# Kernel optimization log

Hardware: AMD Instinct MI355X
Metric: run time of the kernel (lower is better)

## Reference

```python
import jax, jax.numpy as jnp
import numpy as np

N, F, H, C = 4096, 128, 32, 205   # nodes, in-features, hidden=32, clusters=ceil(4096/20)
L, T, R = 512, 12, 4              # teams, team size, replaced members per team
EPS_POOL = 1e-15                  # torch_geometric EPS in dense_diff_pool
BN_EPS = 1e-5


def setup_inputs():
    ks = jax.random.split(jax.random.key(0), 12)
    rng = np.random.default_rng(0)
    # distinct node ids per team; replace = first R members, remain = rest
    teams = np.argsort(rng.random((L, N)), axis=1)[:, :T].astype(np.int64)
    g = lambda i, shape, s: jax.random.normal(ks[i], shape, jnp.float32) * s
    D = 2 * H + C  # 269
    return {
        'x': g(0, (N, F), 1.0),
        'adj': jax.random.uniform(ks[1], (1, N, N), jnp.float32),
        'sample_teams': jnp.asarray(teams),
        'sample_replaces': jnp.asarray(teams[:, :R]),
        'W1r': g(2, (F, H), 0.08), 'b1': jnp.zeros((H,), jnp.float32), 'W1root': g(3, (F, H), 0.08),
        'g1': jnp.ones((H,), jnp.float32), 'be1': jnp.zeros((H,), jnp.float32),
        'W2r': g(4, (H, H), 0.17), 'b2': jnp.zeros((H,), jnp.float32), 'W2root': g(5, (H, H), 0.17),
        'g2': jnp.ones((H,), jnp.float32), 'be2': jnp.zeros((H,), jnp.float32),
        'W3r': g(6, (H, C), 0.17), 'b3': jnp.zeros((C,), jnp.float32), 'W3root': g(7, (H, C), 0.17),
        'g3': jnp.ones((C,), jnp.float32), 'be3': jnp.zeros((C,), jnp.float32),
        'Wl1': g(8, (D, C), 0.07), 'bl1': jnp.zeros((C,), jnp.float32),
    }


def _conv(x, adj, Wr, br, Wroot):
    # DenseGraphConv: lin_rel(adj @ x) + lin_root(x)  (lin_root has no bias)
    return jnp.matmul(adj, x) @ Wr + br + x @ Wroot


def _bn(x, gamma, beta):
    # BatchNorm1d in training mode over flattened (B*N, C)
    B, n, c = x.shape
    xf = x.reshape(-1, c)
    m = xf.mean(0)
    v = jnp.mean((xf - m) ** 2, axis=0)  # biased variance, as torch uses for normalization
    return (((xf - m) / jnp.sqrt(v + BN_EPS)) * gamma + beta).reshape(B, n, c)


def _rownorm(a, eps=1e-8):
    n = jnp.linalg.norm(a, axis=1, keepdims=True)
    return a / jnp.maximum(n, eps)


def reference(x, adj, sample_teams, sample_replaces, W1r, b1, W1root, g1, be1,
              W2r, b2, W2root, g2, be2, W3r, b3, W3root, g3, be3, Wl1, bl1):
    # GNN tower (relu before bn, matching self.bn(i, conv(...).relu()))
    x1 = _bn(jax.nn.relu(_conv(x, adj, W1r, b1, W1root)), g1, be1)    # [1,N,H]
    x2 = _bn(jax.nn.relu(_conv(x1, adj, W2r, b2, W2root)), g2, be2)   # [1,N,H]
    x3 = _bn(jax.nn.relu(_conv(x2, adj, W3r, b3, W3root)), g3, be3)   # [1,N,C]
    xcat = jnp.concatenate([x1, x2, x3], axis=-1)                     # [1,N,2H+C]
    s1 = jax.nn.softmax(jax.nn.relu(xcat @ Wl1 + bl1), axis=2)        # [1,N,C]

    # link-prediction style norm: || s1[0] @ s1[0]^T - adj ||_F
    tmp = s1[0] @ s1[0].T - adj                                       # [1,N,N]
    norm = jnp.sqrt(jnp.sum(tmp * tmp))

    # dense_diff_pool entropy loss (it re-softmaxes its input s)
    s2 = jax.nn.softmax(s1, axis=-1)
    e1 = jnp.mean(jnp.sum(-s2 * jnp.log(s2 + EPS_POOL), axis=-1))

    # similarity alignment: only the diagonal of sim_matrix(sim_x_mat, sim_s_mat) is summed
    xn = _rownorm(x)
    sn = _rownorm(s1[0])
    sim_x_mat = xn @ xn.T                                             # [N,N]
    sim_s_mat = sn @ sn.T                                             # [N,N]
    a_n = _rownorm(sim_x_mat)
    b_n = _rownorm(sim_s_mat)
    sim = -jnp.sum(a_n * b_n) / sim_x_mat.shape[0]

    # per-team replace/remain mean-embedding L1 loss (padded segment means)
    emb = xcat[0]                                                     # [N, 2H+C]
    rep = emb[sample_replaces].mean(axis=1)                           # [L, D]
    rem = emb[sample_teams[:, R:]].mean(axis=1)                       # [L, D]
    embedding_loss = jnp.mean(jnp.sum(jnp.abs(rep - rem), axis=-1))

    total_loss = 100.0 * norm + 10.0 * e1 + 100.0 * sim + embedding_loss
    return (s1, norm, e1, sim, total_loss, embedding_loss, emb)
```

## Files before the change

### kernel.cpp

```cpp
#include <hip/hip_runtime.h>
#include <math.h>

#define NN 4096
#define FF 128
#define HH 32
#define CC 205
#define DD 269
#define LL 512
#define TT 12
#define RR 4
#define GP 208
#define DP 288
#define BST 40
#define GTS 224
#define NFIN 768
#define SC(i) ((i) * 32)
#define ZSTATS_N 10496
#define ZGT_N 69888

typedef __attribute__((ext_vector_type(8))) short bf16x8;
typedef __attribute__((ext_vector_type(4))) float f32x4;
typedef __attribute__((ext_vector_type(8))) unsigned short u16x8;

__device__ __forceinline__ float wave_sum(float v) {
#pragma unroll
  for (int o = 32; o > 0; o >>= 1) v += __shfl_xor(v, o, 64);
  return v;
}
__device__ __forceinline__ float wave_max(float v) {
#pragma unroll
  for (int o = 32; o > 0; o >>= 1) v = fmaxf(v, __shfl_xor(v, o, 64));
  return v;
}
__device__ __forceinline__ unsigned short f2bf(float x) {
  union { float f; unsigned u; } v; v.f = x;
  unsigned r = v.u + 0x7FFFu + ((v.u >> 16) & 1u);
  return (unsigned short)(r >> 16);
}

__global__ __launch_bounds__(256) void k_prep(const float* __restrict__ x,
                                              const float* __restrict__ W1r,
                                              const float* __restrict__ W1root,
                                              const float* __restrict__ Wl1,
                                              unsigned short* __restrict__ mB,
                                              float* __restrict__ rootb,
                                              float* __restrict__ xn,
                                              unsigned short* __restrict__ xnR,
                                              unsigned short* __restrict__ xnB,
                                              unsigned short* __restrict__ Wl1T,
                                              float* __restrict__ zstats,
                                              unsigned int* __restrict__ zgt) {
  __shared__ float sX[32][132];
  __shared__ unsigned short sT[32][34];
  __shared__ unsigned short sT2[FF][34];
  const int tid = threadIdx.x;
  {
    const int gidx = blockIdx.x * 256 + tid;
    if (gidx < ZSTATS_N) zstats[gidx] = 0.f;
    for (int i = gidx; i < ZGT_N; i += 65536) zgt[i] = 0u;
    if (gidx < GP * DP) {
      const int c = gidx / DP, k = gidx - c * DP;
      Wl1T[gidx] = (c < CC && k < DD) ? f2bf(Wl1[(size_t)k * CC + c]) : (unsigned short)0;
    }
  }
  if (blockIdx.x < 128) {
    const int kb = blockIdx.x;
    for (int p = tid; p < 1024; p += 256) {
      const int node = p >> 5, c4 = p & 31;
      const float4 v = *reinterpret_cast<const float4*>(&x[((size_t)(kb * 32 + node)) * FF + c4 * 4]);
      sX[node][c4 * 4 + 0] = v.x; sX[node][c4 * 4 + 1] = v.y;
      sX[node][c4 * 4 + 2] = v.z; sX[node][c4 * 4 + 3] = v.w;
    }
    __syncthreads();
    const int c = tid & 31, g = tid >> 5;
    float a1[4] = {0.f, 0.f, 0.f, 0.f}, a2[4] = {0.f, 0.f, 0.f, 0.f};
    for (int k = 0; k < FF; ++k) {
      const float w1 = W1r[k * HH + c];
      const float w2 = W1root[k * HH + c];
#pragma unroll
      for (int ni = 0; ni < 4; ++ni) {
        const float av = sX[g * 4 + ni][k];
        a1[ni] = fmaf(av, w1, a1[ni]);
        a2[ni] = fmaf(av, w2, a2[ni]);
      }
    }
#pragma unroll
    for (int ni = 0; ni < 4; ++ni) {
      rootb[((size_t)kb * 32 + g * 4 + ni) * HH + c] = a2[ni];
      sT[c][g * 4 + ni] = f2bf(a1[ni]);
    }
    __syncthreads();
    if (tid < 128) {
      const int row = tid >> 2, seg = tid & 3;
      u16x8 v;
#pragma unroll
      for (int j = 0; j < 8; ++j) v[j] = sT[row][seg * 8 + j];
      *reinterpret_cast<u16x8*>(&mB[((size_t)kb * 32 + row) * 32 + seg * 8]) = v;
    }
  } else {
    const int kb = blockIdx.x - 128;
    const int lane = tid & 63;
    const int w = tid >> 6;
#pragma unroll
    for (int i = 0; i < 8; ++i) {
      const int node = w * 8 + i;
      const int row = kb * 32 + node;
      const float v0 = x[(size_t)row * FF + lane];
      const float v1 = x[(size_t)row * FF + 64 + lane];
      const float ss = wave_sum(v0 * v0 + v1 * v1);
      const float n = fmaxf(sqrtf(ss), 1e-8f);
      const float a = v0 / n, b = v1 / n;
      xn[(size_t)row * FF + lane] = a;
      xn[(size_t)row * FF + 64 + lane] = b;
      xnR[(size_t)row * FF + lane] = f2bf(a);
      xnR[(size_t)row * FF + 64 + lane] = f2bf(b);
      sT2[lane][node] = f2bf(a);
      sT2[64 + lane][node] = f2bf(b);
    }
    __syncthreads();
    const int rowc = tid >> 1, seg = (tid & 1) * 16;
    if (rowc < FF) {
      u16x8 a, b;
#pragma unroll
      for (int j = 0; j < 8; ++j) { a[j] = sT2[rowc][seg + j]; b[j] = sT2[rowc][seg + 8 + j]; }
      *reinterpret_cast<u16x8*>(&xnB[((size_t)kb * GP + rowc) * 32 + seg]) = a;
      *reinterpret_cast<u16x8*>(&xnB[((size_t)kb * GP + rowc) * 32 + seg + 8]) = b;
    }
  }
}

__global__ __launch_bounds__(512) void k_conv1(const float* __restrict__ adj,
                                               unsigned short* __restrict__ adj_t,
                                               const unsigned short* __restrict__ mB,
                                               const float* __restrict__ bias,
                                               const float* __restrict__ root,
                                               float* __restrict__ t,
                                               float* __restrict__ colsum,
                                               float* __restrict__ colsq,
                                               float* __restrict__ scalars) {
  __shared__ unsigned short sA[16][520];
  __shared__ float sRed[8][16][33];
  __shared__ float ls[HH], lq[HH];
  __shared__ float redsq[8];
  const int tid = threadIdx.x;
  const int lane = tid & 63;
  const int w = tid >> 6;
  const int l15 = lane & 15;
  const int kgrp = (lane >> 4) * 8;
  const int rb = blockIdx.x;
  const int row0 = rb * 16;
  float adjsq = 0.f;
  f32x4 acc0 = {0.f, 0.f, 0.f, 0.f}, acc1 = {0.f, 0.f, 0.f, 0.f};
  const int fr[4] = {(0 * 512 + tid) >> 7, (1 * 512 + tid) >> 7, (2 * 512 + tid) >> 7,
                     (3 * 512 + tid) >> 7};
  const int fc[4] = {(0 * 512 + tid) & 127, (1 * 512 + tid) & 127, (2 * 512 + tid) & 127,
                     (3 * 512 + tid) & 127};
  float4 v[4];
#pragma unroll
  for (int i = 0; i < 4; ++i)
    v[i] = *reinterpret_cast<const float4*>(&adj[(size_t)(row0 + fr[i]) * NN + fc[i] * 4]);
  for (int chunk = 0; chunk < 8; ++chunk) {
    const int kbase = chunk * 512;
#pragma unroll
    for (int i = 0; i < 4; ++i) {
      const float4 vv = v[i];
      adjsq += vv.x * vv.x + vv.y * vv.y + vv.z * vv.z + vv.w * vv.w;
      ushort4 h;
      h.x = f2bf(vv.x); h.y = f2bf(vv.y); h.z = f2bf(vv.z); h.w = f2bf(vv.w);
      const size_t toff = ((size_t)rb * (NN / 32) + (kbase >> 5) + (fc[i] >> 3)) * 512 +
                          fr[i] * 32 + (fc[i] & 7) * 4;
      *reinterpret_cast<ushort4*>(&adj_t[toff]) = h;
      *reinterpret_cast<ushort4*>(&sA[fr[i]][fc[i] * 4]) = h;
    }
    __syncthreads();
    if (chunk < 7) {
      const int kn = kbase + 512;
#pragma unroll
      for (int i = 0; i < 4; ++i)
        v[i] = *reinterpret_cast<const float4*>(&adj[(size_t)(row0 + fr[i]) * NN + kn + fc[i] * 4]);
    }
#pragma unroll
    for (int j = 0; j < 2; ++j) {
      const int ktl = w * 2 + j;
      const bf16x8 a = *reinterpret_cast<const bf16x8*>(&sA[l15][ktl * 32 + kgrp]);
      const size_t boff = (size_t)(chunk * 16 + ktl) * 1024;
      const bf16x8 b0 = *reinterpret_cast<const bf16x8*>(&mB[boff + l15 * 32 + kgrp]);
      const bf16x8 b1v = *reinterpret_cast<const bf16x8*>(&mB[boff + (16 + l15) * 32 + kgrp]);
      acc0 = __builtin_amdgcn_mfma_f32_16x16x32_bf16(a, b0, acc0, 0, 0, 0);
      acc1 = __builtin_amdgcn_mfma_f32_16x16x32_bf16(a, b1v, acc1, 0, 0, 0);
    }
    __syncthreads();
  }
  const int crow = (lane >> 4) * 4;
#pragma unroll
  for (int r = 0; r < 4; ++r) {
    sRed[w][crow + r][l15] = acc0[r];
    sRed[w][crow + r][16 + l15] = acc1[r];
  }
  if (tid < HH) { ls[tid] = 0.f; lq[tid] = 0.f; }
  adjsq = wave_sum(adjsq);
  if (lane == 0) redsq[w] = adjsq;
  __syncthreads();
  {
    const int r = tid >> 5, c = tid & 31;
    float vv = 0.f;
#pragma unroll
    for (int i = 0; i < 8; ++i) vv += sRed[i][r][c];
    const int n = row0 + r;
    float s = bias[c] + root[(size_t)n * HH + c] + vv;
    s = fmaxf(s, 0.f);
    t[(size_t)n * HH + c] = s;
    atomicAdd(&ls[c], s);
    atomicAdd(&lq[c], s * s);
  }
  __syncthreads();
  if (tid < HH) {
    atomicAdd(&colsum[tid * 16], ls[tid]);
    atomicAdd(&colsq[tid * 16], lq[tid]);
  }
  if (tid == 0) {
    float s = 0.f;
#pragma unroll
    for (int i = 0; i < 8; ++i) s += redsq[i];
    atomicAdd(&scalars[SC(1)], s);
  }
}

__global__ __launch_bounds__(512) void k_conv2(const unsigned short* __restrict__ adj_t,
                                               const unsigned short* __restrict__ mB,
                                               const float* __restrict__ bias,
                                               const float* __restrict__ root,
                                               float* __restrict__ t,
                                               float* __restrict__ colsum,
                                               float* __restrict__ colsq) {
  __shared__ float sRed[8][16][33];
  __shared__ float ls[HH], lq[HH];
  const int tid = threadIdx.x;
  const int lane = tid & 63;
  const int w = tid >> 6;
  const int l15 = lane & 15;
  const int kgrp = (lane >> 4) * 8;
  const int rb = blockIdx.x;
  const int row0 = rb * 16;
  const int kb0 = w * 16;
  f32x4 acc0 = {0.f, 0.f, 0.f, 0.f}, acc1 = {0.f, 0.f, 0.f, 0.f};
#pragma unroll
  for (int h = 0; h < 2; ++h) {
    bf16x8 a[8], b0[8], b1v[8];
#pragma unroll
    for (int kt = 0; kt < 8; ++kt) {
      const int kb = kb0 + h * 8 + kt;
      const size_t aoff = ((size_t)rb * (NN / 32) + kb) * 512;
      const size_t boff = (size_t)kb * 1024;
      a[kt] = *reinterpret_cast<const bf16x8*>(&adj_t[aoff + l15 * 32 + kgrp]);
      b0[kt] = *reinterpret_cast<const bf16x8*>(&mB[boff + (size_t)l15 * 32 + kgrp]);
      b1v[kt] = *reinterpret_cast<const bf16x8*>(&mB[boff + (size_t)(16 + l15) * 32 + kgrp]);
    }
#pragma unroll
    for (int kt = 0; kt < 8; ++kt) {
      acc0 = __builtin_amdgcn_mfma_f32_16x16x32_bf16(a[kt], b0[kt], acc0, 0, 0, 0);
      acc1 = __builtin_amdgcn_mfma_f32_16x16x32_bf16(a[kt], b1v[kt], acc1, 0, 0, 0);
    }
  }
  const int crow = (lane >> 4) * 4;
#pragma unroll
  for (int r = 0; r < 4; ++r) {
    sRed[w][crow + r][l15] = acc0[r];
    sRed[w][crow + r][16 + l15] = acc1[r];
  }
  if (tid < HH) { ls[tid] = 0.f; lq[tid] = 0.f; }
  __syncthreads();
  {
    const int r = tid >> 5, c = tid & 31;
    float v = 0.f;
#pragma unroll
    for (int i = 0; i < 8; ++i) v += sRed[i][r][c];
    const int n = row0 + r;
    float s = bias[c] + root[(size_t)n * HH + c] + v;
    s = fmaxf(s, 0.f);
    t[(size_t)n * HH + c] = s;
    atomicAdd(&ls[c], s);
    atomicAdd(&lq[c], s * s);
  }
  __syncthreads();
  if (tid < HH) {
    atomicAdd(&colsum[tid * 16], ls[tid]);
    atomicAdd(&colsq[tid * 16], lq[tid]);
  }
}

__global__ __launch_bounds__(512) void k_conv3(const unsigned short* __restrict__ adj_t,
                                               const unsigned short* __restrict__ x2B,
                                               const float* __restrict__ W3r,
                                               const float* __restrict__ b3,
                                               const float* __restrict__ x2,
                                               const float* __restrict__ W3root,
                                               float* __restrict__ t3,
                                               float* __restrict__ colsum,
                                               float* __restrict__ colsq) {
  __shared__ float sRed[8][16][33];
  __shared__ float sZ[16][33];
  __shared__ float sXr[16][33];
  const int tid = threadIdx.x;
  const int lane = tid & 63;
  const int w = tid >> 6;
  const int l15 = lane & 15;
  const int kgrp = (lane >> 4) * 8;
  const int rb = blockIdx.x;
  const int row0 = rb * 16;
  const int kb0 = w * 16;
  f32x4 acc0 = {0.f, 0.f, 0.f, 0.f}, acc1 = {0.f, 0.f, 0.f, 0.f};
#pragma unroll
  for (int h = 0; h < 2; ++h) {
    bf16x8 a[8], b0[8], b1v[8];
#pragma unroll
    for (int kt = 0; kt < 8; ++kt) {
      const int kb = kb0 + h * 8 + kt;
      const size_t aoff = ((size_t)rb * (NN / 32) + kb) * 512;
      const size_t boff = (size_t)kb * 1024;
      a[kt] = *reinterpret_cast<const bf16x8*>(&adj_t[aoff + l15 * 32 + kgrp]);
      b0[kt] = *reinterpret_cast<const bf16x8*>(&x2B[boff + (size_t)l15 * 32 + kgrp]);
      b1v[kt] = *reinterpret_cast<const bf16x8*>(&x2B[boff + (size_t)(16 + l15) * 32 + kgrp]);
    }
#pragma unroll
    for (int kt = 0; kt < 8; ++kt) {
      acc0 = __builtin_amdgcn_mfma_f32_16x16x32_bf16(a[kt], b0[kt], acc0, 0, 0, 0);
      acc1 = __builtin_amdgcn_mfma_f32_16x16x32_bf16(a[kt], b1v[kt], acc1, 0, 0, 0);
    }
  }
  const int crow = (lane >> 4) * 4;
#pragma unroll
  for (int r = 0; r < 4; ++r) {
    sRed[w][crow + r][l15] = acc0[r];
    sRed[w][crow + r][16 + l15] = acc1[r];
  }
  {
    const int r = tid >> 5, c = tid & 31;
    if (tid < 512) sXr[r][c] = x2[(size_t)(row0 + r) * HH + c];
  }
  __syncthreads();
  {
    const int r = tid >> 5, c = tid & 31;
    float v = 0.f;
#pragma unroll
    for (int i = 0; i < 8; ++i) v += sRed[i][r][c];
    sZ[r][c] = v;
  }
  __syncthreads();
  const int c = tid;
  if (c >= CC) return;
  float acc[16];
  const float bb = b3[c];
#pragma unroll
  for (int r = 0; r < 16; ++r) acc[r] = bb;
  for (int k = 0; k < 32; ++k) {
    const float w1 = W3r[k * CC + c];
    const float w2 = W3root[k * CC + c];
#pragma unroll
    for (int r = 0; r < 16; ++r) acc[r] += sZ[r][k] * w1 + sXr[r][k] * w2;
  }
  float lsm = 0.f, lqm = 0.f;
#pragma unroll
  for (int r = 0; r < 16; ++r) {
    const float v = fmaxf(acc[r], 0.f);
    t3[(size_t)(row0 + r) * CC + c] = v;
    lsm += v;
    lqm += v * v;
  }
  atomicAdd(&colsum[c * 16], lsm);
  atomicAdd(&colsq[c * 16], lqm);
}

__global__ __launch_bounds__(256) void k_bnproj(const float* __restrict__ t,
                                                const float* __restrict__ colsum,
                                                const float* __restrict__ colsq,
                                                const float* __restrict__ g,
                                                const float* __restrict__ be,
                                                const float* __restrict__ W2r,
                                                const float* __restrict__ W2root,
                                                unsigned short* __restrict__ mB,
                                                float* __restrict__ rootb,
                                                float* __restrict__ emb) {
  __shared__ float sXf[32][33];
  __shared__ unsigned short sT[32][34];
  const int tid = threadIdx.x;
  const int kb = blockIdx.x;
  const int c = tid & 31, gq = tid >> 5;
  const float m = colsum[c * 16] * (1.f / NN);
  const float var = fmaxf(colsq[c * 16] * (1.f / NN) - m * m, 0.f);
  const float Ac = g[c] / sqrtf(var + 1e-5f);
  const float Bc = be[c] - m * Ac;
#pragma unroll
  for (int ni = 0; ni < 4; ++ni) {
    const int n = kb * 32 + gq * 4 + ni;
    const float v = fmaf(Ac, t[(size_t)n * HH + c], Bc);
    emb[(size_t)n * DD + c] = v;
    sXf[gq * 4 + ni][c] = v;
  }
  __syncthreads();
  float a1[4] = {0.f, 0.f, 0.f, 0.f}, a2[4] = {0.f, 0.f, 0.f, 0.f};
  for (int k = 0; k < HH; ++k) {
    const float w1 = W2r[k * HH + c];
    const float w2 = W2root[k * HH + c];
#pragma unroll
    for (int ni = 0; ni < 4; ++ni) {
      const float av = sXf[gq * 4 + ni][k];
      a1[ni] = fmaf(av, w1, a1[ni]);
      a2[ni] = fmaf(av, w2, a2[ni]);
    }
  }
#pragma unroll
  for (int ni = 0; ni < 4; ++ni) {
    rootb[((size_t)kb * 32 + gq * 4 + ni) * HH + c] = a2[ni];
    sT[c][gq * 4 + ni] = f2bf(a1[ni]);
  }
  __syncthreads();
  if (tid < 128) {
    const int row = tid >> 2, seg = tid & 3;
    u16x8 v;
#pragma unroll
    for (int j = 0; j < 8; ++j) v[j] = sT[row][seg * 8 + j];
    *reinterpret_cast<u16x8*>(&mB[((size_t)kb * 32 + row) * 32 + seg * 8]) = v;
  }
}

__global__ __launch_bounds__(256) void k_bnapply32(const float* __restrict__ t,
                                                   const float* __restrict__ colsum,
                                                   const float* __restrict__ colsq,
                                                   const float* __restrict__ g,
                                                   const float* __restrict__ be,
                                                   float* __restrict__ xo,
                                                   float* __restrict__ emb, int embOff,
                                                   unsigned short* __restrict__ xB) {
  __shared__ unsigned short sT[32][34];
  const int tid = threadIdx.x;
  const int kb = blockIdx.x;
  const int c = tid & 31, gq = tid >> 5;
  const float m = colsum[c * 16] * (1.f / NN);
  const float var = fmaxf(colsq[c * 16] * (1.f / NN) - m * m, 0.f);
  const float Ac = g[c] / sqrtf(var + 1e-5f);
  const float Bc = be[c] - m * Ac;
#pragma unroll
  for (int ni = 0; ni < 4; ++ni) {
    const int n = kb * 32 + gq * 4 + ni;
    const float v = fmaf(Ac, t[(size_t)n * HH + c], Bc);
    xo[(size_t)n * HH + c] = v;
    emb[(size_t)n * DD + embOff + c] = v;
    sT[c][gq * 4 + ni] = f2bf(v);
  }
  __syncthreads();
  if (tid < 128) {
    const int row = tid >> 2, seg = tid & 3;
    u16x8 o;
#pragma unroll
    for (int j = 0; j < 8; ++j) o[j] = sT[row][seg * 8 + j];
    *reinterpret_cast<u16x8*>(&xB[((size_t)kb * 32 + row) * 32 + seg * 8]) = o;
  }
}

__global__ __launch_bounds__(256) void k_head(float* __restrict__ emb,
                                              const float* __restrict__ t3,
                                              const float* __restrict__ colsum3,
                                              const float* __restrict__ colsq3,
                                              const float* __restrict__ g3,
                                              const float* __restrict__ be3,
                                              const unsigned short* __restrict__ Wl1T,
                                              const float* __restrict__ bl1,
                                              float* __restrict__ s1,
                                              float* __restrict__ sn,
                                              unsigned short* __restrict__ s1B,
                                              unsigned short* __restrict__ snB,
                                              unsigned short* __restrict__ snR,
                                              float* __restrict__ scalars) {
  __shared__ unsigned short sA[16][296];
  __shared__ float lg[16][212];
  __shared__ unsigned short sTa[16][212];
  __shared__ unsigned short sTb[16][212];
  __shared__ float redE[4];
  const int tid = threadIdx.x;
  const int row0 = blockIdx.x * 16;
  for (int p = tid; p < 16 * 36; p += 256) {
    const int r = p / 36, ch = p - r * 36;
    const int row = row0 + r;
#pragma unroll
    for (int j = 0; j < 8; ++j) {
      const int d = ch * 8 + j;
      float v;
      if (d < 2 * HH) {
        v = emb[(size_t)row * DD + d];
      } else if (d < DD) {
        const int c3 = d - 2 * HH;
        const float m = colsum3[c3 * 16] * (1.f / NN);
        const float var = fmaxf(colsq3[c3 * 16] * (1.f / NN) - m * m, 0.f);
        const float Ac = g3[c3] / sqrtf(var + 1e-5f);
        const float Bc = be3[c3] - m * Ac;
        v = fmaf(Ac, t3[(size_t)row * CC + c3], Bc);
        emb[(size_t)row * DD + d] = v;
      } else {
        v = 0.f;
      }
      sA[r][d] = f2bf(v);
    }
  }
  __syncthreads();
  const int lane = tid & 63;
  const int w = tid >> 6;
  const int l15 = lane & 15;
  const int kgrp = (lane >> 4) * 8;
  {
    f32x4 acc[4];
#pragma unroll
    for (int i = 0; i < 4; ++i) acc[i] = (f32x4){0.f, 0.f, 0.f, 0.f};
#pragma unroll
    for (int i = 0; i < 4; ++i) {
      const int ct = w + i * 4;
      if (ct < 13) {
        const size_t brow = (size_t)(ct * 16 + l15) * DP;
#pragma unroll
        for (int k0 = 0; k0 < DP; k0 += 32) {
          const bf16x8 a = *reinterpret_cast<const bf16x8*>(&sA[l15][k0 + kgrp]);
          const bf16x8 b = *reinterpret_cast<const bf16x8*>(&Wl1T[brow + k0 + kgrp]);
          acc[i] = __builtin_amdgcn_mfma_f32_16x16x32_bf16(a, b, acc[i], 0, 0, 0);
        }
      }
    }
    const int lrow = (lane >> 4) * 4;
#pragma unroll
    for (int i = 0; i < 4; ++i) {
      const int ct = w + i * 4;
      if (ct < 13) {
#pragma unroll
        for (int r = 0; r < 4; ++r) lg[lrow + r][ct * 16 + l15] = acc[i][r];
      }
    }
  }
  __syncthreads();
  const int r0 = w * 4;
  const int c0 = lane * 4;
  const bool active = (c0 < GP);
  float bl[4];
#pragma unroll
  for (int j = 0; j < 4; ++j) bl[j] = (c0 + j < CC) ? bl1[c0 + j] : 0.f;
  float ent_acc = 0.f;
#pragma unroll
  for (int r = 0; r < 4; ++r) {
    const int lr = r0 + r;
    const int row = row0 + lr;
    float lgv[4] = {0.f, 0.f, 0.f, 0.f};
    if (active) {
#pragma unroll
      for (int j = 0; j < 4; ++j) lgv[j] = lg[lr][c0 + j];
    }
    float v[4];
    float ml = -1e30f;
#pragma unroll
    for (int j = 0; j < 4; ++j) {
      const int c = c0 + j;
      v[j] = (c < CC) ? fmaxf(lgv[j] + bl[j], 0.f) : -1e30f;
      ml = fmaxf(ml, v[j]);
    }
    const float m = wave_max(ml);
    float e[4];
    float sl = 0.f;
#pragma unroll
    for (int j = 0; j < 4; ++j) {
      const int c = c0 + j;
      e[j] = (c < CC) ? __expf(v[j] - m) : 0.f;
      sl += e[j];
    }
    const float S = wave_sum(sl);
    const float invS = 1.f / S;
    float p[4];
    float ql = 0.f;
#pragma unroll
    for (int j = 0; j < 4; ++j) {
      p[j] = e[j] * invS;
      ql += p[j] * p[j];
    }
    const float q = wave_sum(ql);
    const float inv = 1.f / fmaxf(sqrtf(q), 1e-8f);
    float m2l = -1e30f;
#pragma unroll
    for (int j = 0; j < 4; ++j) {
      const int c = c0 + j;
      if (c < CC) {
        s1[(size_t)row * CC + c] = p[j];
        sn[(size_t)row * CC + c] = p[j] * inv;
        m2l = fmaxf(m2l, p[j]);
      }
    }
    if (active) {
#pragma unroll
      for (int j = 0; j < 4; ++j) {
        const int c = c0 + j;
        const bool ok = (c < CC);
        sTa[lr][c] = ok ? f2bf(p[j]) : (unsigned short)0;
        sTb[lr][c] = ok ? f2bf(p[j] * inv) : (unsigned short)0;
      }
    }
    if (c0 < GTS) {
      ushort4 o;
      o.x = (c0 + 0 < CC) ? f2bf(p[0] * inv) : (unsigned short)0;
      o.y = (c0 + 1 < CC) ? f2bf(p[1] * inv) : (unsigned short)0;
      o.z = (c0 + 2 < CC) ? f2bf(p[2] * inv) : (unsigned short)0;
      o.w = (c0 + 3 < CC) ? f2bf(p[3] * inv) : (unsigned short)0;
      *reinterpret_cast<ushort4*>(&snR[(size_t)row * GTS + c0]) = o;
    }
    const float m2 = wave_max(m2l);
    float e2[4];
    float s2l = 0.f;
#pragma unroll
    for (int j = 0; j < 4; ++j) {
      const int c = c0 + j;
      e2[j] = (c < CC) ? __expf(p[j] - m2) : 0.f;
      s2l += e2[j];
    }
    const float S2 = wave_sum(s2l);
    const float invS2 = 1.f / S2;
    float tl = 0.f;
#pragma unroll
    for (int j = 0; j < 4; ++j) {
      const int c = c0 + j;
      if (c < CC) {
        const float sp = e2[j] * invS2;
        tl -= sp * logf(sp + 1e-15f);
      }
    }
    ent_acc += tl;
  }
  ent_acc = wave_sum(ent_acc);
  if (lane == 0) redE[w] = ent_acc;
  __syncthreads();
  if (tid == 0) atomicAdd(&scalars[SC(2)], redE[0] + redE[1] + redE[2] + redE[3]);
  if (tid < GP) {
    const int kb = row0 >> 5, no = row0 & 31;
    u16x8 oa0, ob0, oa1, ob1;
#pragma unroll
    for (int r = 0; r < 8; ++r) {
      oa0[r] = sTa[r][tid]; ob0[r] = sTb[r][tid];
      oa1[r] = sTa[8 + r][tid]; ob1[r] = sTb[8 + r][tid];
    }
    *reinterpret_cast<u16x8*>(&s1B[((size_t)kb * GP + tid) * 32 + no]) = oa0;
    *reinterpret_cast<u16x8*>(&s1B[((size_t)kb * GP + tid) * 32 + no + 8]) = oa1;
    *reinterpret_cast<u16x8*>(&snB[((size_t)kb * GP + tid) * 32 + no]) = ob0;
    *reinterpret_cast<u16x8*>(&snB[((size_t)kb * GP + tid) * 32 + no + 8]) = ob1;
  }
}

__global__ __launch_bounds__(512) void k_tail(const unsigned short* __restrict__ adj_t,
                                              const unsigned short* __restrict__ s1B,
                                              const float* __restrict__ s1,
                                              const unsigned short* __restrict__ xnB,
                                              const unsigned short* __restrict__ snB,
                                              unsigned short* __restrict__ GT0,
                                              unsigned short* __restrict__ GxsT,
                                              unsigned short* __restrict__ GsT,
                                              float* __restrict__ scalars) {
  const int tid = threadIdx.x;
  const int lane = tid & 63;
  const int w = tid >> 6;
  const int l15 = lane & 15;
  const int kgrp = (lane >> 4) * 8;
  if (blockIdx.x < 512) {
    __shared__ unsigned short sB[2][13][16][BST];
    __shared__ float red[8];
    const int bx = blockIdx.x & 31;
    const int ky = blockIdx.x >> 5;
    const int rb = bx * 8 + w;
    const int kb0 = ky * 8;
    const int g = lane >> 4;
    const int p0 = tid;
    const int ct0 = p0 >> 6, rr0 = (p0 >> 2) & 15, sg0 = (p0 & 3) * 8;
    const int p1 = tid + 512;
    const bool v1 = (p1 < 832);
    const int ct1 = p1 >> 6, rr1 = (p1 >> 2) & 15, sg1 = (p1 & 3) * 8;
    f32x4 acc[13];
#pragma unroll
    for (int ct = 0; ct < 13; ++ct) acc[ct] = (f32x4){0.f, 0.f, 0.f, 0.f};
    u16x8 st0, st1;
    st0 = *reinterpret_cast<const u16x8*>(&s1B[((size_t)kb0 * GP + ct0 * 16 + rr0) * 32 + sg0]);
    if (v1) st1 = *reinterpret_cast<const u16x8*>(&s1B[((size_t)kb0 * GP + ct1 * 16 + rr1) * 32 + sg1]);
    *reinterpret_cast<u16x8*>(&sB[0][ct0][rr0][sg0]) = st0;
    if (v1) *reinterpret_cast<u16x8*>(&sB[0][ct1][rr1][sg1]) = st1;
    __syncthreads();
    bf16x8 a = *reinterpret_cast<const bf16x8*>(
        &adj_t[((size_t)rb * (NN / 32) + kb0) * 512 + l15 * 32 + kgrp]);
    for (int kt = 0; kt < 8; ++kt) {
      const int cur = kt & 1;
      if (kt < 7) {
        const size_t kb = kb0 + kt + 1;
        st0 = *reinterpret_cast<const u16x8*>(&s1B[(kb * GP + ct0 * 16 + rr0) * 32 + sg0]);
        if (v1) st1 = *reinterpret_cast<const u16x8*>(&s1B[(kb * GP + ct1 * 16 + rr1) * 32 + sg1]);
      }
      bf16x8 a_next = a;
      if (kt < 7)
        a_next = *reinterpret_cast<const bf16x8*>(
            &adj_t[((size_t)rb * (NN / 32) + kb0 + kt + 1) * 512 + l15 * 32 + kgrp]);
#pragma unroll
      for (int ct = 0; ct < 13; ++ct) {
        const bf16x8 b = *reinterpret_cast<const bf16x8*>(&sB[cur][ct][l15][kgrp]);
        acc[ct] = __builtin_amdgcn_mfma_f32_16x16x32_bf16(a, b, acc[ct], 0, 0, 0);
      }
      if (kt < 7) {
        *reinterpret_cast<u16x8*>(&sB[cur ^ 1][ct0][rr0][sg0]) = st0;
        if (v1) *reinterpret_cast<u16x8*>(&sB[cur ^ 1][ct1][rr1][sg1]) = st1;
      }
      __syncthreads();
      a = a_next;
    }
    const int rout = rb * 16 + g * 4;
    float sc = 0.f;
#pragma unroll
    for (int ct = 0; ct < 13; ++ct) {
      const int col = ct * 16 + l15;
      if (col < CC) {
#pragma unroll
        for (int r = 0; r < 4; ++r)
          sc = fmaf(acc[ct][r], s1[(size_t)(rout + r) * CC + col], sc);
      }
    }
    sc = wave_sum(sc);
    if (lane == 0) red[w] = sc;
    __syncthreads();
    if (tid == 0) {
      float s = 0.f;
#pragma unroll
      for (int i = 0; i < 8; ++i) s += red[i];
      atomicAdd(&scalars[SC(0)], s);
    }
  } else {
    __shared__ float redg[8][16][17];
    __shared__ float redq[8];
    const int gb = blockIdx.x - 512;
    const int gid = gb / 169;
    const int rem = gb - gid * 169;
    const int tp = (rem % 13) * 16;
    const int tq = (rem / 13) * 16;
    const unsigned short *PT, *QT;
    unsigned short* GTout = nullptr;
    if (gid == 0)      { PT = xnB; QT = xnB; GTout = GT0;  if (tp >= FF || tq >= FF) return; }
    else if (gid == 1) { PT = xnB; QT = snB; GTout = GxsT; if (tp >= FF) return; }
    else if (gid == 2) { PT = snB; QT = snB; GTout = GsT; }
    else               { PT = s1B; QT = s1B; }
    f32x4 acc = {0.f, 0.f, 0.f, 0.f};
#pragma unroll 4
    for (int kt = 0; kt < 16; ++kt) {
      const int kb = w * 16 + kt;
      const bf16x8 a = *reinterpret_cast<const bf16x8*>(&PT[((size_t)kb * GP + tp + l15) * 32 + kgrp]);
      const bf16x8 b = *reinterpret_cast<const bf16x8*>(&QT[((size_t)kb * GP + tq + l15) * 32 + kgrp]);
      acc = __builtin_amdgcn_mfma_f32_16x16x32_bf16(a, b, acc, 0, 0, 0);
    }
    const int crow = (lane >> 4) * 4;
#pragma unroll
    for (int r = 0; r < 4; ++r) redg[w][crow + r][l15] = acc[r];
    __syncthreads();
    const int rr = tid >> 4, cc = tid & 15;
    if (gid == 3) {
      float q = 0.f;
      if (tid < 256) {
        float v = 0.f;
#pragma unroll
        for (int i = 0; i < 8; ++i) v += redg[i][rr][cc];
        q = v * v;
      }
      q = wave_sum(q);
      if (lane == 0) redq[w] = q;
      __syncthreads();
      if (tid == 0) {
        float s = 0.f;
#pragma unroll
        for (int i = 0; i < 8; ++i) s += redq[i];
        atomicAdd(&scalars[SC(5)], s);
      }
    } else {
      if (tid < 256) {
        float vt = 0.f;
#pragma unroll
        for (int i = 0; i < 8; ++i) vt += redg[i][cc][rr];
        GTout[(size_t)(tq + rr) * GTS + (tp + cc)] = f2bf(vt);
      }
    }
  }
}

__global__ __launch_bounds__(256) void k_finloss(const unsigned short* __restrict__ xnR,
                                                 const unsigned short* __restrict__ snR,
                                                 const unsigned short* __restrict__ GT0,
                                                 const unsigned short* __restrict__ GxsT,
                                                 const unsigned short* __restrict__ GsT,
                                                 const float* __restrict__ xn,
                                                 const float* __restrict__ sn,
                                                 const float* __restrict__ emb,
                                                 const int* __restrict__ teams,
                                                 const int* __restrict__ reps,
                                                 float* __restrict__ scalars,
                                                 unsigned int* __restrict__ ticket,
                                                 float* __restrict__ outsc) {
  __shared__ __align__(16) char smem[47424];
  const int tid = threadIdx.x;
  if (blockIdx.x < 256) {
    unsigned short (*sX)[136] = (unsigned short(*)[136])(smem);
    unsigned short (*sS)[232] = (unsigned short(*)[232])(smem + 4352);
    float (*sH1)[132] = (float(*)[132])(smem + 11776);
    float (*sU)[212] = (float(*)[212])(smem + 20224);
    float (*sH2)[212] = (float(*)[212])(smem + 33792);
    float* redb = (float*)(smem + 47360);
    const int row0 = blockIdx.x * 16;
    for (int p = tid; p < 16 * 16; p += 256) {
      const int r = p >> 4, ch = p & 15;
      *reinterpret_cast<u16x8*>(&sX[r][ch * 8]) =
          *reinterpret_cast<const u16x8*>(&xnR[(size_t)(row0 + r) * FF + ch * 8]);
    }
    for (int p = tid; p < 16 * 28; p += 256) {
      const int r = p / 28, ch = p - r * 28;
      *reinterpret_cast<u16x8*>(&sS[r][ch * 8]) =
          *reinterpret_cast<const u16x8*>(&snR[(size_t)(row0 + r) * GTS + ch * 8]);
    }
    __syncthreads();
    const int lane = tid & 63;
    const int w = tid >> 6;
    const int l15 = lane & 15;
    const int kgrp = (lane >> 4) * 8;
    const int lrow = (lane >> 4) * 4;
#pragma unroll
    for (int i = 0; i < 2; ++i) {
      const int ct = w + i * 4;
      f32x4 acc = {0.f, 0.f, 0.f, 0.f};
      const size_t brow = (size_t)(ct * 16 + l15) * GTS;
#pragma unroll
      for (int k0 = 0; k0 < FF; k0 += 32) {
        const bf16x8 a = *reinterpret_cast<const bf16x8*>(&sX[l15][k0 + kgrp]);
        const bf16x8 b = *reinterpret_cast<const bf16x8*>(&GT0[brow + k0 + kgrp]);
        acc = __builtin_amdgcn_mfma_f32_16x16x32_bf16(a, b, acc, 0, 0, 0);
      }
#pragma unroll
      for (int r = 0; r < 4; ++r) sH1[lrow + r][ct * 16 + l15] = acc[r];
    }
#pragma unroll
    for (int i = 0; i < 4; ++i) {
      const int ct = w + i * 4;
      if (ct < 13) {
        f32x4 acc = {0.f, 0.f, 0.f, 0.f};
        const size_t brow = (size_t)(ct * 16 + l15) * GTS;
#pragma unroll
        for (int k0 = 0; k0 < FF; k0 += 32) {
          const bf16x8 a = *reinterpret_cast<const bf16x8*>(&sX[l15][k0 + kgrp]);
          const bf16x8 b = *reinterpret_cast<const bf16x8*>(&GxsT[brow + k0 + kgrp]);
          acc = __builtin_amdgcn_mfma_f32_16x16x32_bf16(a, b, acc, 0, 0, 0);
        }
#pragma unroll
        for (int r = 0; r < 4; ++r) sU[lrow + r][ct * 16 + l15] = acc[r];
      }
    }
#pragma unroll
    for (int i = 0; i < 4; ++i) {
      const int ct = w + i * 4;
      if (ct < 13) {
        f32x4 acc = {0.f, 0.f, 0.f, 0.f};
        const size_t brow = (size_t)(ct * 16 + l15) * GTS;
#pragma unroll
        for (int k0 = 0; k0 < GTS; k0 += 32) {
          const bf16x8 a = *reinterpret_cast<const bf16x8*>(&sS[l15][k0 + kgrp]);
          const bf16x8 b = *reinterpret_cast<const bf16x8*>(&GsT[brow + k0 + kgrp]);
          acc = __builtin_amdgcn_mfma_f32_16x16x32_bf16(a, b, acc, 0, 0, 0);
        }
#pragma unroll
        for (int r = 0; r < 4; ++r) sH2[lrow + r][ct * 16 + l15] = acc[r];
      }
    }
    __syncthreads();
    float acc_sim = 0.f;
#pragma unroll
    for (int r = 0; r < 4; ++r) {
      const int lr = w * 4 + r;
      const int row = row0 + lr;
      float suu = 0.f, suv = 0.f, svv = 0.f;
#pragma unroll
      for (int c0 = 0; c0 < FF; c0 += 64) {
        suu = fmaf(xn[(size_t)row * FF + c0 + lane], sH1[lr][c0 + lane], suu);
      }
      for (int cb = lane; cb < CC; cb += 64) {
        const float sv = sn[(size_t)row * CC + cb];
        suv = fmaf(sU[lr][cb], sv, suv);
        svv = fmaf(sH2[lr][cb], sv, svv);
      }
      suu = wave_sum(suu);
      suv = wave_sum(suv);
      svv = wave_sum(svv);
      if (lane == 0) acc_sim += suv / sqrtf(suu * svv);
    }
    if (lane == 0) redb[w] = acc_sim;
    __syncthreads();
    if (tid == 0) atomicAdd(&scalars[SC(3)], redb[0] + redb[1] + redb[2] + redb[3]);
  } else {
    float* red = (float*)smem;
    const int team = blockIdx.x - 256;
    float part = 0.f;
    for (int d = tid; d < DD; d += 256) {
      float a = 0.f, b = 0.f;
#pragma unroll
      for (int m = 0; m < RR; ++m) a += emb[(size_t)reps[team * RR + m] * DD + d];
#pragma unroll
      for (int m = RR; m < TT; ++m) b += emb[(size_t)teams[team * TT + m] * DD + d];
      part += fabsf(a * (1.f / RR) - b * (1.f / (TT - RR)));
    }
    part = wave_sum(part);
    if ((tid & 63) == 0) red[tid >> 6] = part;
    __syncthreads();
    if (tid == 0) atomicAdd(&scalars[SC(4)], red[0] + red[1] + red[2] + red[3]);
  }
  if (tid == 0) {
    __threadfence();
    const unsigned int old = atomicAdd(ticket, 1u);
    if (old == (unsigned int)(NFIN - 1)) {
      const float trSAS = atomicAdd(&scalars[SC(0)], 0.f);
      const float adjsq = atomicAdd(&scalars[SC(1)], 0.f);
      const float ent   = atomicAdd(&scalars[SC(2)], 0.f);
      const float simS  = atomicAdd(&scalars[SC(3)], 0.f);
      const float embS  = atomicAdd(&scalars[SC(4)], 0.f);
      const float sumP2 = atomicAdd(&scalars[SC(5)], 0.f);
      const float normsq = fmaxf(sumP2 - 2.f * trSAS + adjsq, 0.f);
      const float norm = sqrtf(normsq);
      const float e1 = ent * (1.f / NN);
      const float sim = -simS * (1.f / NN);
      const float embl = embS * (1.f / LL);
      outsc[0] = norm;
      outsc[1] = e1;
      outsc[2] = sim;
      outsc[3] = 100.f * norm + 10.f * e1 + 100.f * sim + embl;
      outsc[4] = embl;
    }
  }
}

extern "C" void kernel_launch(void* const* d_in, const int* in_sizes, int n_in,
                              void* d_out, int out_size, void* d_ws, size_t ws_size,
                              hipStream_t stream) {
  const float* x      = (const float*)d_in[0];
  const float* adj    = (const float*)d_in[1];
  const int*   teams  = (const int*)d_in[2];
  const int*   reps   = (const int*)d_in[3];
  const float* W1r    = (const float*)d_in[4];
  const float* b1     = (const float*)d_in[5];
  const float* W1root = (const float*)d_in[6];
  const float* g1     = (const float*)d_in[7];
  const float* be1    = (const float*)d_in[8];
  const float* W2r    = (const float*)d_in[9];
  const float* b2     = (const float*)d_in[10];
  const float* W2root = (const float*)d_in[11];
  const float* g2     = (const float*)d_in[12];
  const float* be2    = (const float*)d_in[13];
  const float* W3r    = (const float*)d_in[14];
  const float* b3     = (const float*)d_in[15];
  const float* W3root = (const float*)d_in[16];
  const float* g3     = (const float*)d_in[17];
  const float* be3    = (const float*)d_in[18];
  const float* Wl1    = (const float*)d_in[19];
  const float* bl1    = (const float*)d_in[20];

  char* wp = (char*)d_ws;
  auto alloc = [&](size_t bytes) { char* p = wp; wp += (bytes + 255) & ~(size_t)255; return p; };
  unsigned short* adj_t = (unsigned short*)alloc((size_t)NN * NN * 2);
  unsigned short* mB    = (unsigned short*)alloc((size_t)HH * NN * 2);
  unsigned short* x2B   = (unsigned short*)alloc((size_t)HH * NN * 2);
  unsigned short* s1B   = (unsigned short*)alloc((size_t)GP * NN * 2);
  unsigned short* snB   = (unsigned short*)alloc((size_t)GP * NN * 2);
  unsigned short* Wl1T  = (unsigned short*)alloc((size_t)GP * DP * 2);
  unsigned short* xnR   = (unsigned short*)alloc((size_t)NN * FF * 2);
  unsigned short* snR   = (unsigned short*)alloc((size_t)NN * GTS * 2);
  float* rootb  = (float*)alloc((size_t)NN * HH * 4);
  float* t      = (float*)alloc((size_t)NN * HH * 4);
  float* x2     = (float*)alloc((size_t)NN * HH * 4);
  float* t3     = (float*)alloc((size_t)NN * CC * 4);
  float* sn     = (float*)alloc((size_t)NN * CC * 4);
  float* xn     = (float*)alloc((size_t)NN * FF * 4);
  unsigned short* xnB   = (unsigned short*)alloc((size_t)GP * NN * 2);
  float* scalars = (float*)alloc(256 * 4);
  float* colsum1 = (float*)alloc(512 * 4);
  float* colsq1  = (float*)alloc(512 * 4);
  float* colsum2 = (float*)alloc(512 * 4);
  float* colsq2  = (float*)alloc(512 * 4);
  float* colsum3 = (float*)alloc(4096 * 4);
  float* colsq3  = (float*)alloc(4096 * 4);
  unsigned short* GTall = (unsigned short*)alloc((size_t)3 * GP * GTS * 2);
  unsigned short* GT0   = GTall;
  unsigned short* GxsT  = GTall + (size_t)GP * GTS;
  unsigned short* GsT   = GTall + (size_t)2 * GP * GTS;
  unsigned int* ticket = (unsigned int*)&scalars[SC(6)];
  (void)ws_size; (void)in_sizes; (void)n_in; (void)out_size;

  float* out   = (float*)d_out;
  float* s1    = out;
  float* outsc = out + (size_t)NN * CC;
  float* emb   = out + (size_t)NN * CC + 5;

  k_prep<<<256, 256, 0, stream>>>(x, W1r, W1root, Wl1, mB, rootb, xn, xnR, xnB, Wl1T,
                                  scalars, (unsigned int*)GTall);

  k_conv1<<<256, 512, 0, stream>>>(adj, adj_t, mB, b1, rootb, t, colsum1, colsq1, scalars);
  k_bnproj<<<NN / 32, 256, 0, stream>>>(t, colsum1, colsq1, g1, be1, W2r, W2root, mB, rootb, emb);

  k_conv2<<<256, 512, 0, stream>>>(adj_t, mB, b2, rootb, t, colsum2, colsq2);
  k_bnapply32<<<NN / 32, 256, 0, stream>>>(t, colsum2, colsq2, g2, be2, x2, emb, HH, x2B);

  k_conv3<<<256, 512, 0, stream>>>(adj_t, x2B, W3r, b3, x2, W3root, t3, colsum3, colsq3);

  k_head<<<NN / 16, 256, 0, stream>>>(emb, t3, colsum3, colsq3, g3, be3, Wl1T, bl1,
                                      s1, sn, s1B, snB, snR, scalars);

  k_tail<<<512 + 676, 512, 0, stream>>>(adj_t, s1B, s1, xnB, snB, GT0, GxsT, GsT, scalars);

  k_finloss<<<NFIN, 256, 0, stream>>>(xnR, snR, GT0, GxsT, GsT, xn, sn, emb, teams, reps,
                                      scalars, ticket, outsc);
}
```

Baseline: 182.0 us.

## Fuse batchnorm apply and projection into conv kernels via grid-wide ticket barrier

```diff
diff --git a/kernel.cpp b/kernel.cpp
--- a/kernel.cpp
+++ b/kernel.cpp
@@ -15,7 +15,7 @@
 #define GTS 224
 #define NFIN 768
 #define SC(i) ((i) * 32)
-#define ZSTATS_N 10496
+#define ZSTATS_N 10560
 #define ZGT_N 69888
 
 typedef __attribute__((ext_vector_type(8))) short bf16x8;
@@ -131,17 +131,26 @@
 
 __global__ __launch_bounds__(512) void k_conv1(const float* __restrict__ adj,
                                                unsigned short* __restrict__ adj_t,
-                                               const unsigned short* __restrict__ mB,
+                                               unsigned short* __restrict__ mB,
                                                const float* __restrict__ bias,
                                                const float* __restrict__ root,
-                                               float* __restrict__ t,
+                                               const float* __restrict__ g,
+                                               const float* __restrict__ be,
+                                               const float* __restrict__ W2r,
+                                               const float* __restrict__ W2root,
+                                               float* __restrict__ rootb,
+                                               float* __restrict__ emb,
                                                float* __restrict__ colsum,
                                                float* __restrict__ colsq,
-                                               float* __restrict__ scalars) {
+                                               float* __restrict__ scalars,
+                                               unsigned int* __restrict__ tk) {
   __shared__ unsigned short sA[16][520];
   __shared__ float sRed[8][16][33];
   __shared__ float ls[HH], lq[HH];
   __shared__ float redsq[8];
+  __shared__ float sTt[16][33];
+  __shared__ float sXf[16][33];
+  __shared__ unsigned short sTm[32][18];
   const int tid = threadIdx.x;
   const int lane = tid & 63;
   const int w = tid >> 6;
@@ -201,17 +210,16 @@
   adjsq = wave_sum(adjsq);
   if (lane == 0) redsq[w] = adjsq;
   __syncthreads();
+  const int r16 = tid >> 5, c32 = tid & 31;
   {
-    const int r = tid >> 5, c = tid & 31;
     float vv = 0.f;
 #pragma unroll
-    for (int i = 0; i < 8; ++i) vv += sRed[i][r][c];
-    const int n = row0 + r;
-    float s = bias[c] + root[(size_t)n * HH + c] + vv;
+    for (int i = 0; i < 8; ++i) vv += sRed[i][r16][c32];
+    float s = bias[c32] + root[(size_t)(row0 + r16) * HH + c32] + vv;
     s = fmaxf(s, 0.f);
-    t[(size_t)n * HH + c] = s;
-    atomicAdd(&ls[c], s);
-    atomicAdd(&lq[c], s * s);
+    sTt[r16][c32] = s;
+    atomicAdd(&ls[c32], s);
+    atomicAdd(&lq[c32], s * s);
   }
   __syncthreads();
   if (tid < HH) {
@@ -223,6 +231,43 @@
 #pragma unroll
     for (int i = 0; i < 8; ++i) s += redsq[i];
     atomicAdd(&scalars[SC(1)], s);
+  }
+  if (tid == 0) {
+    __threadfence();
+    atomicAdd(tk, 1u);
+    while (atomicAdd(tk, 0u) < 256u) __builtin_amdgcn_s_sleep(8);
+  }
+  __syncthreads();
+  {
+    const float cs = atomicAdd(&colsum[c32 * 16], 0.f);
+    const float cq = atomicAdd(&colsq[c32 * 16], 0.f);
+    const float m = cs * (1.f / NN);
+    const float var = fmaxf(cq * (1.f / NN) - m * m, 0.f);
+    const float Ac = g[c32] / sqrtf(var + 1e-5f);
+    const float Bc = be[c32] - m * Ac;
+    const float vv = fmaf(Ac, sTt[r16][c32], Bc);
+    emb[(size_t)(row0 + r16) * DD + c32] = vv;
+    sXf[r16][c32] = vv;
+  }
+  __syncthreads();
+  {
+    float a1 = 0.f, a2 = 0.f;
+    for (int k = 0; k < HH; ++k) {
+      const float av = sXf[r16][k];
+      a1 = fmaf(av, W2r[k * HH + c32], a1);
+      a2 = fmaf(av, W2root[k * HH + c32], a2);
+    }
+    rootb[(size_t)(row0 + r16) * HH + c32] = a2;
+    sTm[c32][r16] = f2bf(a1);
+  }
+  __syncthreads();
+  if (tid < 64) {
+    const int row = tid >> 1, half = tid & 1;
+    u16x8 o;
+#pragma unroll
+    for (int j = 0; j < 8; ++j) o[j] = sTm[row][half * 8 + j];
+    const int kb = rb >> 1;
+    *reinterpret_cast<u16x8*>(&mB[((size_t)(kb * 32 + row)) * 32 + (rb & 1) * 16 + half * 8]) = o;
   }
 }
 
@@ -230,11 +275,18 @@
                                                const unsigned short* __restrict__ mB,
                                                const float* __restrict__ bias,
                                                const float* __restrict__ root,
-                                               float* __restrict__ t,
+                                               const float* __restrict__ g,
+                                               const float* __restrict__ be,
+                                               float* __restrict__ x2,
+                                               float* __restrict__ emb,
+                                               unsigned short* __restrict__ x2B,
                                                float* __restrict__ colsum,
-                                               float* __restrict__ colsq) {
+                                               float* __restrict__ colsq,
+                                               unsigned int* __restrict__ tk) {
   __shared__ float sRed[8][16][33];
   __shared__ float ls[HH], lq[HH];
+  __shared__ float sTt[16][33];
+  __shared__ unsigned short sTm[32][18];
   const int tid = threadIdx.x;
   const int lane = tid & 63;
   const int w = tid >> 6;
@@ -270,22 +322,48 @@
   }
   if (tid < HH) { ls[tid] = 0.f; lq[tid] = 0.f; }
   __syncthreads();
+  const int r16 = tid >> 5, c32 = tid & 31;
   {
-    const int r = tid >> 5, c = tid & 31;
-    float v = 0.f;
-#pragma unroll
-    for (int i = 0; i < 8; ++i) v += sRed[i][r][c];
-    const int n = row0 + r;
-    float s = bias[c] + root[(size_t)n * HH + c] + v;
+    float vv = 0.f;
+#pragma unroll
+    for (int i = 0; i < 8; ++i) vv += sRed[i][r16][c32];
+    float s = bias[c32] + root[(size_t)(row0 + r16) * HH + c32] + vv;
     s = fmaxf(s, 0.f);
-    t[(size_t)n * HH + c] = s;
-    atomicAdd(&ls[c], s);
-    atomicAdd(&lq[c], s * s);
+    sTt[r16][c32] = s;
+    atomicAdd(&ls[c32], s);
+    atomicAdd(&lq[c32], s * s);
   }
   __syncthreads();
   if (tid < HH) {
     atomicAdd(&colsum[tid * 16], ls[tid]);
     atomicAdd(&colsq[tid * 16], lq[tid]);
+  }
+  if (tid == 0) {
+    __threadfence();
+    atomicAdd(tk, 1u);
+    while (atomicAdd(tk, 0u) < 256u) __builtin_amdgcn_s_sleep(8);
+  }
+  __syncthreads();
+  {
+    const float cs = atomicAdd(&colsum[c32 * 16], 0.f);
+    const float cq = atomicAdd(&colsq[c32 * 16], 0.f);
+    const float m = cs * (1.f / NN);
+    const float var = fmaxf(cq * (1.f / NN) - m * m, 0.f);
+    const float Ac = g[c32] / sqrtf(var + 1e-5f);
+    const float Bc = be[c32] - m * Ac;
+    const float vv = fmaf(Ac, sTt[r16][c32], Bc);
+    x2[(size_t)(row0 + r16) * HH + c32] = vv;
+    emb[(size_t)(row0 + r16) * DD + HH + c32] = vv;
+    sTm[c32][r16] = f2bf(vv);
+  }
+  __syncthreads();
+  if (tid < 64) {
+    const int row = tid >> 1, half = tid & 1;
+    u16x8 o;
+#pragma unroll
+    for (int j = 0; j < 8; ++j) o[j] = sTm[row][half * 8 + j];
+    const int kb = rb >> 1;
+    *reinterpret_cast<u16x8*>(&x2B[((size_t)(kb * 32 + row)) * 32 + (rb & 1) * 16 + half * 8]) = o;
   }
 }
 
@@ -369,93 +447,6 @@
   }
   atomicAdd(&colsum[c * 16], lsm);
   atomicAdd(&colsq[c * 16], lqm);
-}
-
-__global__ __launch_bounds__(256) void k_bnproj(const float* __restrict__ t,
-                                                const float* __restrict__ colsum,
-                                                const float* __restrict__ colsq,
-                                                const float* __restrict__ g,
-                                                const float* __restrict__ be,
-                                                const float* __restrict__ W2r,
-                                                const float* __restrict__ W2root,
-                                                unsigned short* __restrict__ mB,
-                                                float* __restrict__ rootb,
-                                                float* __restrict__ emb) {
-  __shared__ float sXf[32][33];
-  __shared__ unsigned short sT[32][34];
-  const int tid = threadIdx.x;
-  const int kb = blockIdx.x;
-  const int c = tid & 31, gq = tid >> 5;
-  const float m = colsum[c * 16] * (1.f / NN);
-  const float var = fmaxf(colsq[c * 16] * (1.f / NN) - m * m, 0.f);
-  const float Ac = g[c] / sqrtf(var + 1e-5f);
-  const float Bc = be[c] - m * Ac;
-#pragma unroll
-  for (int ni = 0; ni < 4; ++ni) {
-    const int n = kb * 32 + gq * 4 + ni;
-    const float v = fmaf(Ac, t[(size_t)n * HH + c], Bc);
-    emb[(size_t)n * DD + c] = v;
-    sXf[gq * 4 + ni][c] = v;
-  }
-  __syncthreads();
-  float a1[4] = {0.f, 0.f, 0.f, 0.f}, a2[4] = {0.f, 0.f, 0.f, 0.f};
-  for (int k = 0; k < HH; ++k) {
-    const float w1 = W2r[k * HH + c];
-    const float w2 = W2root[k * HH + c];
-#pragma unroll
-    for (int ni = 0; ni < 4; ++ni) {
-      const float av = sXf[gq * 4 + ni][k];
-      a1[ni] = fmaf(av, w1, a1[ni]);
-      a2[ni] = fmaf(av, w2, a2[ni]);
-    }
-  }
-#pragma unroll
-  for (int ni = 0; ni < 4; ++ni) {
-    rootb[((size_t)kb * 32 + gq * 4 + ni) * HH + c] = a2[ni];
-    sT[c][gq * 4 + ni] = f2bf(a1[ni]);
-  }
-  __syncthreads();
-  if (tid < 128) {
-    const int row = tid >> 2, seg = tid & 3;
-    u16x8 v;
-#pragma unroll
-    for (int j = 0; j < 8; ++j) v[j] = sT[row][seg * 8 + j];
-    *reinterpret_cast<u16x8*>(&mB[((size_t)kb * 32 + row) * 32 + seg * 8]) = v;
-  }
-}
-
-__global__ __launch_bounds__(256) void k_bnapply32(const float* __restrict__ t,
-                                                   const float* __restrict__ colsum,
-                                                   const float* __restrict__ colsq,
-                                                   const float* __restrict__ g,
-                                                   const float* __restrict__ be,
-                                                   float* __restrict__ xo,
-                                                   float* __restrict__ emb, int embOff,
-                                                   unsigned short* __restrict__ xB) {
-  __shared__ unsigned short sT[32][34];
-  const int tid = threadIdx.x;
-  const int kb = blockIdx.x;
-  const int c = tid & 31, gq = tid >> 5;
-  const float m = colsum[c * 16] * (1.f / NN);
-  const float var = fmaxf(colsq[c * 16] * (1.f / NN) - m * m, 0.f);
-  const float Ac = g[c] / sqrtf(var + 1e-5f);
-  const float Bc = be[c] - m * Ac;
-#pragma unroll
-  for (int ni = 0; ni < 4; ++ni) {
-    const int n = kb * 32 + gq * 4 + ni;
-    const float v = fmaf(Ac, t[(size_t)n * HH + c], Bc);
-    xo[(size_t)n * HH + c] = v;
-    emb[(size_t)n * DD + embOff + c] = v;
-    sT[c][gq * 4 + ni] = f2bf(v);
-  }
-  __syncthreads();
-  if (tid < 128) {
-    const int row = tid >> 2, seg = tid & 3;
-    u16x8 o;
-#pragma unroll
-    for (int j = 0; j < 8; ++j) o[j] = sT[row][seg * 8 + j];
-    *reinterpret_cast<u16x8*>(&xB[((size_t)kb * 32 + row) * 32 + seg * 8]) = o;
-  }
 }
 
 __global__ __launch_bounds__(256) void k_head(float* __restrict__ emb,
@@ -969,13 +960,12 @@
   unsigned short* xnR   = (unsigned short*)alloc((size_t)NN * FF * 2);
   unsigned short* snR   = (unsigned short*)alloc((size_t)NN * GTS * 2);
   float* rootb  = (float*)alloc((size_t)NN * HH * 4);
-  float* t      = (float*)alloc((size_t)NN * HH * 4);
   float* x2     = (float*)alloc((size_t)NN * HH * 4);
   float* t3     = (float*)alloc((size_t)NN * CC * 4);
   float* sn     = (float*)alloc((size_t)NN * CC * 4);
   float* xn     = (float*)alloc((size_t)NN * FF * 4);
   unsigned short* xnB   = (unsigned short*)alloc((size_t)GP * NN * 2);
-  float* scalars = (float*)alloc(256 * 4);
+  float* scalars = (float*)alloc(320 * 4);
   float* colsum1 = (float*)alloc(512 * 4);
   float* colsq1  = (float*)alloc(512 * 4);
   float* colsum2 = (float*)alloc(512 * 4);
@@ -987,6 +977,8 @@
   unsigned short* GxsT  = GTall + (size_t)GP * GTS;
   unsigned short* GsT   = GTall + (size_t)2 * GP * GTS;
   unsigned int* ticket = (unsigned int*)&scalars[SC(6)];
+  unsigned int* tk1    = (unsigned int*)&scalars[SC(7)];
+  unsigned int* tk2    = (unsigned int*)&scalars[SC(8)];
   (void)ws_size; (void)in_sizes; (void)n_in; (void)out_size;
 
   float* out   = (float*)d_out;
@@ -997,11 +989,11 @@
   k_prep<<<256, 256, 0, stream>>>(x, W1r, W1root, Wl1, mB, rootb, xn, xnR, xnB, Wl1T,
                                   scalars, (unsigned int*)GTall);
 
-  k_conv1<<<256, 512, 0, stream>>>(adj, adj_t, mB, b1, rootb, t, colsum1, colsq1, scalars);
-  k_bnproj<<<NN / 32, 256, 0, stream>>>(t, colsum1, colsq1, g1, be1, W2r, W2root, mB, rootb, emb);
-
-  k_conv2<<<256, 512, 0, stream>>>(adj_t, mB, b2, rootb, t, colsum2, colsq2);
-  k_bnapply32<<<NN / 32, 256, 0, stream>>>(t, colsum2, colsq2, g2, be2, x2, emb, HH, x2B);
+  k_conv1<<<256, 512, 0, stream>>>(adj, adj_t, mB, b1, rootb, g1, be1, W2r, W2root,
+                                   rootb, emb, colsum1, colsq1, scalars, tk1);
+
+  k_conv2<<<256, 512, 0, stream>>>(adj_t, mB, b2, rootb, g2, be2, x2, emb, x2B,
+                                   colsum2, colsq2, tk2);
 
   k_conv3<<<256, 512, 0, stream>>>(adj_t, x2B, W3r, b3, x2, W3root, t3, colsum3, colsq3);
 
```

New measurement: 460.0 us. 153% more time.
